# Performance work log

Hardware: AMD Instinct MI355X
Metric: run time of the kernel (lower is better)

## Reference

```python
import jax, jax.numpy as jnp
import numpy as np

# SigNet forward: time-augment -> depth-3 path signature (basepoint=True, via
# Chen's identity over per-segment tensor exponentials) -> Linear. dropout p=0.

B, L, CIN, OUT = 256, 256, 8, 128
C = CIN + 1                      # +1 time channel from signatory.Augment
SIG_CH = C + C**2 + C**3         # signatory.signature_channels(C, depth=3) = 819


def setup_inputs() -> dict:
    key = jax.random.key(0)
    k1, k2, k3 = jax.random.split(key, 3)
    inp = jax.random.normal(k1, (B, L, CIN), dtype=jnp.float32)
    W = jax.random.normal(k2, (SIG_CH, OUT), dtype=jnp.float32) / np.sqrt(SIG_CH).astype(np.float32)
    b = jax.random.normal(k3, (OUT,), dtype=jnp.float32) * 0.01
    return {"inp": inp, "W": W, "b": b}


def _chen(a, bb):
    # Chen's identity for truncated tensor algebra (depth 3):
    # (a*b)_k = sum_{i+j=k} a_i (x) b_j  (with a_0 = b_0 = 1)
    a1, a2, a3 = a
    b1, b2, b3 = bb
    c1 = a1 + b1
    c2 = a2 + b2 + jnp.einsum('...i,...j->...ij', a1, b1)
    c3 = (a3 + b3
          + jnp.einsum('...ij,...k->...ijk', a2, b1)
          + jnp.einsum('...i,...jk->...ijk', a1, b2))
    return (c1, c2, c3)


def _signature_depth3(path):
    # path: [B, L, C]; basepoint=True -> prepend the zero point before diffing
    Bn, Ln, Cn = path.shape
    path = jnp.concatenate([jnp.zeros((Bn, 1, Cn), path.dtype), path], axis=1)
    dx = jnp.moveaxis(jnp.diff(path, axis=1), 1, 0)  # [L, B, C] increments
    # Tensor exponential of each linear segment: exp(dx)_k = dx^{(x)k} / k!
    e1 = dx
    e2 = 0.5 * jnp.einsum('lbi,lbj->lbij', dx, dx)
    e3 = jnp.einsum('lbij,lbk->lbijk', e2, dx) / 3.0  # = dx^(x)3 / 6
    s1, s2, s3 = jax.lax.associative_scan(_chen, (e1, e2, e3), axis=0)
    return jnp.concatenate([s1[-1].reshape(Bn, -1),
                            s2[-1].reshape(Bn, -1),
                            s3[-1].reshape(Bn, -1)], axis=-1)  # [B, SIG_CH]


def reference(inp, W, b):
    Bn, Ln, _ = inp.shape
    # signatory.Augment include_time: linspace(0,1,L) channel, placed first
    t = jnp.broadcast_to(jnp.linspace(0.0, 1.0, Ln, dtype=inp.dtype)[None, :, None], (Bn, Ln, 1))
    x = jnp.concatenate([t, inp], axis=-1)  # [B, L, C]
    y = _signature_depth3(x)
    return y @ W + b  # dropout p=0 is identity
```

## Files before the change

kernel.cpp:

```cpp
#include <hip/hip_runtime.h>


#define PAD 260

__global__ __launch_bounds__(512) void signet_fwd(
    const float* __restrict__ inp,
    const float* __restrict__ W,
    const float* __restrict__ bias,
    float* __restrict__ out)
{
    __shared__ __align__(16) float Wt[9][PAD];
    __shared__ __align__(16) float Zt[9][PAD];
    __shared__ __align__(16) float Dt[9][PAD];
    __shared__ __align__(16) float Xt[9][PAD];
    __shared__ float sig[820];
    __shared__ __align__(16) float4 pbuf[16][32];
    __shared__ __align__(16) float4 part3[244];

    const int tid = threadIdx.x;
    const int b   = blockIdx.x;

    {
        const int t = tid & 255;
        const float* rc = inp + (size_t)b * 2048 + (size_t)t * 8;
        if (tid < 256) {
            float4 c0 = *(const float4*)rc;
            float4 p0 = make_float4(0.f, 0.f, 0.f, 0.f);
            float  tp = 0.f;
            if (t > 0) { p0 = *(const float4*)(rc - 8); tp = (float)(t - 1) * (1.0f / 255.0f); }
            float cur[5] = { (float)t * (1.0f / 255.0f), c0.x, c0.y, c0.z, c0.w };
            float prv[5] = { tp, p0.x, p0.y, p0.z, p0.w };
            if (t == 0) cur[0] = 0.0f;
            #pragma unroll
            for (int c = 0; c < 5; ++c) {
                const float d = cur[c] - prv[c];
                Dt[c][t] = d;
                Xt[c][t] = cur[c];
                Wt[c][t] = prv[c] + 0.5f * d;
                Zt[c][t] = 0.5f * prv[c] + d * (1.0f / 6.0f);
            }
        } else {
            float4 c1 = *(const float4*)(rc + 4);
            float4 p1 = make_float4(0.f, 0.f, 0.f, 0.f);
            if (t > 0) p1 = *(const float4*)(rc - 4);
            float cur[4] = { c1.x, c1.y, c1.z, c1.w };
            float prv[4] = { p1.x, p1.y, p1.z, p1.w };
            #pragma unroll
            for (int c = 0; c < 4; ++c) {
                const float d = cur[c] - prv[c];
                Dt[5 + c][t] = d;
                Xt[5 + c][t] = cur[c];
                Wt[5 + c][t] = prv[c] + 0.5f * d;
                Zt[5 + c][t] = 0.5f * prv[c] + d * (1.0f / 6.0f);
            }
        }
    }
    __syncthreads();

    const int  half = tid >> 8;
    const int  lt   = tid & 255;
    const bool own3 = (lt < 243);
    const int  pp = lt / 3;
    const int  mm = lt - pp * 3;
    const int  si = pp / 9;
    const int  sj = pp - si * 9;
    const int  sk = mm * 3;

    float a0 = 0.f, a1 = 0.f, a2 = 0.f, s2a = 0.f;

    if (own3) {
        const int qb = half * 32;
        const float4* w4 = (const float4*)Wt[si] + qb;
        const float4* z4 = (const float4*)Zt[si] + qb;
        const float4* dj = (const float4*)Dt[sj] + qb;
        const float4* x0 = (const float4*)Xt[sk] + qb;
        const float4* x1 = (const float4*)Xt[sk + 1] + qb;
        const float4* x2 = (const float4*)Xt[sk + 2] + qb;
        const float4* d0 = (const float4*)Dt[sk] + qb;
        const float4* d1 = (const float4*)Dt[sk + 1] + qb;
        const float4* d2 = (const float4*)Dt[sk + 2] + qb;

        #pragma unroll 2
        for (int q = 0; q < 32; ++q) {
            const float4 w = w4[q], z = z4[q], dd = dj[q];
            const float4 X0 = x0[q], X1 = x1[q], X2 = x2[q];
            const float4 D0 = d0[q], D1 = d1[q], D2 = d2[q];
            {   const float u = w.x * dd.x, v = z.x * dd.x;  s2a += u;
                a0 = fmaf(v, D0.x, fmaf(-u, X0.x, a0));
                a1 = fmaf(v, D1.x, fmaf(-u, X1.x, a1));
                a2 = fmaf(v, D2.x, fmaf(-u, X2.x, a2)); }
            {   const float u = w.y * dd.y, v = z.y * dd.y;  s2a += u;
                a0 = fmaf(v, D0.y, fmaf(-u, X0.y, a0));
                a1 = fmaf(v, D1.y, fmaf(-u, X1.y, a1));
                a2 = fmaf(v, D2.y, fmaf(-u, X2.y, a2)); }
            {   const float u = w.z * dd.z, v = z.z * dd.z;  s2a += u;
                a0 = fmaf(v, D0.z, fmaf(-u, X0.z, a0));
                a1 = fmaf(v, D1.z, fmaf(-u, X1.z, a1));
                a2 = fmaf(v, D2.z, fmaf(-u, X2.z, a2)); }
            {   const float u = w.w * dd.w, v = z.w * dd.w;  s2a += u;
                a0 = fmaf(v, D0.w, fmaf(-u, X0.w, a0));
                a1 = fmaf(v, D1.w, fmaf(-u, X1.w, a1));
                a2 = fmaf(v, D2.w, fmaf(-u, X2.w, a2)); }
        }
    }

    if (own3 && half) part3[lt] = make_float4(a0, a1, a2, s2a);
    __syncthreads();

    if (own3 && !half) {
        const float4 p = part3[lt];
        a0 += p.x;  a1 += p.y;  a2 += p.z;  s2a += p.w;
        const float xl0 = Xt[sk][255], xl1 = Xt[sk + 1][255], xl2 = Xt[sk + 2][255];
        a0 = fmaf(s2a, xl0, a0);
        a1 = fmaf(s2a, xl1, a1);
        a2 = fmaf(s2a, xl2, a2);
        const int base = 90 + pp * 9 + sk;
        sig[base]     = a0;
        sig[base + 1] = a1;
        sig[base + 2] = a2;
        if (mm == 0) sig[9 + pp] = s2a;
    }
    if (tid < 9) sig[tid] = Xt[tid][255];
    __syncthreads();

    {
        const int oq = tid & 31;
        const int sl = tid >> 5;
        float4 acc = make_float4(0.f, 0.f, 0.f, 0.f);
        const float4* W4 = (const float4*)W;
        for (int ch = sl; ch < 819; ch += 16) {
            const float s = sig[ch];
            const float4 wv = W4[(size_t)ch * 32 + oq];
            acc.x = fmaf(s, wv.x, acc.x);
            acc.y = fmaf(s, wv.y, acc.y);
            acc.z = fmaf(s, wv.z, acc.z);
            acc.w = fmaf(s, wv.w, acc.w);
        }
        pbuf[sl][oq] = acc;
    }
    __syncthreads();
    if (tid < 32) {
        float4 r = pbuf[0][tid];
        #pragma unroll
        for (int s = 1; s < 16; ++s) {
            const float4 p = pbuf[s][tid];
            r.x += p.x; r.y += p.y; r.z += p.z; r.w += p.w;
        }
        const float4 bv = ((const float4*)bias)[tid];
        r.x += bv.x; r.y += bv.y; r.z += bv.z; r.w += bv.w;
        ((float4*)(out + (size_t)b * 128))[tid] = r;
    }
}

extern "C" void kernel_launch(void* const* d_in, const int* in_sizes, int n_in,
                              void* d_out, int out_size, void* d_ws, size_t ws_size,
                              hipStream_t stream) {
    const float* inp  = (const float*)d_in[0];
    const float* Wp   = (const float*)d_in[1];
    const float* bias = (const float*)d_in[2];
    float* outp = (float*)d_out;
    (void)in_sizes; (void)n_in; (void)out_size; (void)d_ws; (void)ws_size;

    hipLaunchKernelGGL(signet_fwd, dim3(256), dim3(512), 0, stream,
                       inp, Wp, bias, outp);
}
```

Baseline: 19.50 us.

## Repartition depth-3 signature work into time chunks with register-blocked j accumulators

Replaces the per-(i,j,k-triple) thread mapping, where each of 243 thread pairs streamed all 256 timesteps, with 16 time chunks of 16 steps. Each of 27 threads per chunk handles one (i, k-triple) and keeps 27+9 register accumulators over all j. The Z and X arrays are no longer stored in shared memory; they are recomputed from W and D, and shared memory is unioned for the partial sums and the linear-layer reduction. The goal is to reuse shared-memory loads across j and cut LDS traffic, at the cost of higher register pressure and an extra cross-chunk reduction pass over 729+81 outputs.

```diff
diff --git a/kernel.cpp b/kernel.cpp
--- a/kernel.cpp
+++ b/kernel.cpp
@@ -1,21 +1,24 @@
 #include <hip/hip_runtime.h>
 
 
-#define PAD 260
+#define ROWF   260
+#define NCHUNK 16
+#define TPC    27
+#define ASTRIDE 29
+#define PART_S2_OFF (NCHUNK * TPC * ASTRIDE)
+#define UNION_FLOATS (PART_S2_OFF + NCHUNK * 81)
 
 __global__ __launch_bounds__(512) void signet_fwd(
     const float* __restrict__ inp,
-    const float* __restrict__ W,
+    const float* __restrict__ Wg,
     const float* __restrict__ bias,
     float* __restrict__ out)
 {
-    __shared__ __align__(16) float Wt[9][PAD];
-    __shared__ __align__(16) float Zt[9][PAD];
-    __shared__ __align__(16) float Dt[9][PAD];
-    __shared__ __align__(16) float Xt[9][PAD];
     __shared__ float sig[820];
-    __shared__ __align__(16) float4 pbuf[16][32];
-    __shared__ __align__(16) float4 part3[244];
+    __shared__ __align__(16) float u[UNION_FLOATS];
+
+    float* Wt = u;
+    float* Dt = u + 9 * ROWF;
 
     const int tid = threadIdx.x;
     const int b   = blockIdx.x;
@@ -30,14 +33,11 @@
             if (t > 0) { p0 = *(const float4*)(rc - 8); tp = (float)(t - 1) * (1.0f / 255.0f); }
             float cur[5] = { (float)t * (1.0f / 255.0f), c0.x, c0.y, c0.z, c0.w };
             float prv[5] = { tp, p0.x, p0.y, p0.z, p0.w };
-            if (t == 0) cur[0] = 0.0f;
             #pragma unroll
             for (int c = 0; c < 5; ++c) {
                 const float d = cur[c] - prv[c];
-                Dt[c][t] = d;
-                Xt[c][t] = cur[c];
-                Wt[c][t] = prv[c] + 0.5f * d;
-                Zt[c][t] = 0.5f * prv[c] + d * (1.0f / 6.0f);
+                Dt[c * ROWF + t] = d;
+                Wt[c * ROWF + t] = prv[c] + 0.5f * d;
             }
         } else {
             float4 c1 = *(const float4*)(rc + 4);
@@ -48,102 +48,147 @@
             #pragma unroll
             for (int c = 0; c < 4; ++c) {
                 const float d = cur[c] - prv[c];
-                Dt[5 + c][t] = d;
-                Xt[5 + c][t] = cur[c];
-                Wt[5 + c][t] = prv[c] + 0.5f * d;
-                Zt[5 + c][t] = 0.5f * prv[c] + d * (1.0f / 6.0f);
+                Dt[(5 + c) * ROWF + t] = d;
+                Wt[(5 + c) * ROWF + t] = prv[c] + 0.5f * d;
             }
         }
     }
     __syncthreads();
 
-    const int  half = tid >> 8;
-    const int  lt   = tid & 255;
-    const bool own3 = (lt < 243);
-    const int  pp = lt / 3;
-    const int  mm = lt - pp * 3;
-    const int  si = pp / 9;
-    const int  sj = pp - si * 9;
-    const int  sk = mm * 3;
-
-    float a0 = 0.f, a1 = 0.f, a2 = 0.f, s2a = 0.f;
-
-    if (own3) {
-        const int qb = half * 32;
-        const float4* w4 = (const float4*)Wt[si] + qb;
-        const float4* z4 = (const float4*)Zt[si] + qb;
-        const float4* dj = (const float4*)Dt[sj] + qb;
-        const float4* x0 = (const float4*)Xt[sk] + qb;
-        const float4* x1 = (const float4*)Xt[sk + 1] + qb;
-        const float4* x2 = (const float4*)Xt[sk + 2] + qb;
-        const float4* d0 = (const float4*)Dt[sk] + qb;
-        const float4* d1 = (const float4*)Dt[sk + 1] + qb;
-        const float4* d2 = (const float4*)Dt[sk + 2] + qb;
-
-        #pragma unroll 2
-        for (int q = 0; q < 32; ++q) {
-            const float4 w = w4[q], z = z4[q], dd = dj[q];
-            const float4 X0 = x0[q], X1 = x1[q], X2 = x2[q];
-            const float4 D0 = d0[q], D1 = d1[q], D2 = d2[q];
-            {   const float u = w.x * dd.x, v = z.x * dd.x;  s2a += u;
-                a0 = fmaf(v, D0.x, fmaf(-u, X0.x, a0));
-                a1 = fmaf(v, D1.x, fmaf(-u, X1.x, a1));
-                a2 = fmaf(v, D2.x, fmaf(-u, X2.x, a2)); }
-            {   const float u = w.y * dd.y, v = z.y * dd.y;  s2a += u;
-                a0 = fmaf(v, D0.y, fmaf(-u, X0.y, a0));
-                a1 = fmaf(v, D1.y, fmaf(-u, X1.y, a1));
-                a2 = fmaf(v, D2.y, fmaf(-u, X2.y, a2)); }
-            {   const float u = w.z * dd.z, v = z.z * dd.z;  s2a += u;
-                a0 = fmaf(v, D0.z, fmaf(-u, X0.z, a0));
-                a1 = fmaf(v, D1.z, fmaf(-u, X1.z, a1));
-                a2 = fmaf(v, D2.z, fmaf(-u, X2.z, a2)); }
-            {   const float u = w.w * dd.w, v = z.w * dd.w;  s2a += u;
-                a0 = fmaf(v, D0.w, fmaf(-u, X0.w, a0));
-                a1 = fmaf(v, D1.w, fmaf(-u, X1.w, a1));
-                a2 = fmaf(v, D2.w, fmaf(-u, X2.w, a2)); }
-        }
-    }
-
-    if (own3 && half) part3[lt] = make_float4(a0, a1, a2, s2a);
-    __syncthreads();
-
-    if (own3 && !half) {
-        const float4 p = part3[lt];
-        a0 += p.x;  a1 += p.y;  a2 += p.z;  s2a += p.w;
-        const float xl0 = Xt[sk][255], xl1 = Xt[sk + 1][255], xl2 = Xt[sk + 2][255];
-        a0 = fmaf(s2a, xl0, a0);
-        a1 = fmaf(s2a, xl1, a1);
-        a2 = fmaf(s2a, xl2, a2);
-        const int base = 90 + pp * 9 + sk;
-        sig[base]     = a0;
-        sig[base + 1] = a1;
-        sig[base + 2] = a2;
-        if (mm == 0) sig[9 + pp] = s2a;
-    }
-    if (tid < 9) sig[tid] = Xt[tid][255];
+    const int  chunk = tid / TPC;
+    const int  tloc  = tid - chunk * TPC;
+    const int  ci    = tloc / 3;
+    const int  kt    = tloc - ci * 3;
+    const bool act   = (chunk < NCHUNK);
+
+    float a[9][3];
+    float s2a[9];
+    #pragma unroll
+    for (int j = 0; j < 9; ++j) { s2a[j] = 0.f; a[j][0] = 0.f; a[j][1] = 0.f; a[j][2] = 0.f; }
+
+    if (act) {
+        const int fb = chunk * 4;
+        const float4* W4 = (const float4*)u;
+        const float4* D4 = (const float4*)u + 9 * 65;
+        const int k0 = 3 * kt;
+
+        #pragma unroll
+        for (int q = 0; q < 4; ++q) {
+            const float4 w  = W4[ci * 65 + fb + q];
+            const float4 di = D4[ci * 65 + fb + q];
+            const float4 Wk0 = W4[(k0 + 0) * 65 + fb + q];
+            const float4 Wk1 = W4[(k0 + 1) * 65 + fb + q];
+            const float4 Wk2 = W4[(k0 + 2) * 65 + fb + q];
+            const float4 Dk0 = D4[(k0 + 0) * 65 + fb + q];
+            const float4 Dk1 = D4[(k0 + 1) * 65 + fb + q];
+            const float4 Dk2 = D4[(k0 + 2) * 65 + fb + q];
+
+            float4 z, X0, X1, X2;
+            z.x = fmaf(-(1.0f / 12.0f), di.x, 0.5f * w.x);
+            z.y = fmaf(-(1.0f / 12.0f), di.y, 0.5f * w.y);
+            z.z = fmaf(-(1.0f / 12.0f), di.z, 0.5f * w.z);
+            z.w = fmaf(-(1.0f / 12.0f), di.w, 0.5f * w.w);
+            X0.x = fmaf(0.5f, Dk0.x, Wk0.x); X0.y = fmaf(0.5f, Dk0.y, Wk0.y);
+            X0.z = fmaf(0.5f, Dk0.z, Wk0.z); X0.w = fmaf(0.5f, Dk0.w, Wk0.w);
+            X1.x = fmaf(0.5f, Dk1.x, Wk1.x); X1.y = fmaf(0.5f, Dk1.y, Wk1.y);
+            X1.z = fmaf(0.5f, Dk1.z, Wk1.z); X1.w = fmaf(0.5f, Dk1.w, Wk1.w);
+            X2.x = fmaf(0.5f, Dk2.x, Wk2.x); X2.y = fmaf(0.5f, Dk2.y, Wk2.y);
+            X2.z = fmaf(0.5f, Dk2.z, Wk2.z); X2.w = fmaf(0.5f, Dk2.w, Wk2.w);
+
+            #pragma unroll
+            for (int j = 0; j < 9; ++j) {
+                const float4 dj = D4[j * 65 + fb + q];
+                { const float uu = w.x * dj.x, vv = z.x * dj.x; s2a[j] += uu;
+                  a[j][0] = fmaf(vv, Dk0.x, fmaf(-uu, X0.x, a[j][0]));
+                  a[j][1] = fmaf(vv, Dk1.x, fmaf(-uu, X1.x, a[j][1]));
+                  a[j][2] = fmaf(vv, Dk2.x, fmaf(-uu, X2.x, a[j][2])); }
+                { const float uu = w.y * dj.y, vv = z.y * dj.y; s2a[j] += uu;
+                  a[j][0] = fmaf(vv, Dk0.y, fmaf(-uu, X0.y, a[j][0]));
+                  a[j][1] = fmaf(vv, Dk1.y, fmaf(-uu, X1.y, a[j][1]));
+                  a[j][2] = fmaf(vv, Dk2.y, fmaf(-uu, X2.y, a[j][2])); }
+                { const float uu = w.z * dj.z, vv = z.z * dj.z; s2a[j] += uu;
+                  a[j][0] = fmaf(vv, Dk0.z, fmaf(-uu, X0.z, a[j][0]));
+                  a[j][1] = fmaf(vv, Dk1.z, fmaf(-uu, X1.z, a[j][1]));
+                  a[j][2] = fmaf(vv, Dk2.z, fmaf(-uu, X2.z, a[j][2])); }
+                { const float uu = w.w * dj.w, vv = z.w * dj.w; s2a[j] += uu;
+                  a[j][0] = fmaf(vv, Dk0.w, fmaf(-uu, X0.w, a[j][0]));
+                  a[j][1] = fmaf(vv, Dk1.w, fmaf(-uu, X1.w, a[j][1]));
+                  a[j][2] = fmaf(vv, Dk2.w, fmaf(-uu, X2.w, a[j][2])); }
+            }
+        }
+    }
+    __syncthreads();
+
+    if (tid < 9) {
+        const float wl = Wt[tid * ROWF + 255];
+        const float dl = Dt[tid * ROWF + 255];
+        sig[tid] = fmaf(0.5f, dl, wl);
+    }
+    __syncthreads();
+
+    if (act) {
+        float* pa = u + (chunk * TPC + tloc) * ASTRIDE;
+        #pragma unroll
+        for (int j = 0; j < 9; ++j) {
+            pa[j * 3 + 0] = a[j][0];
+            pa[j * 3 + 1] = a[j][1];
+            pa[j * 3 + 2] = a[j][2];
+        }
+        if (kt == 0) {
+            float* ps = u + PART_S2_OFF + chunk * 81 + ci * 9;
+            #pragma unroll
+            for (int j = 0; j < 9; ++j) ps[j] = s2a[j];
+        }
+    }
+    __syncthreads();
+
+    if (tid < 81) {
+        float s = 0.f;
+        #pragma unroll
+        for (int c = 0; c < NCHUNK; ++c) s += u[PART_S2_OFF + c * 81 + tid];
+        sig[9 + tid] = s;
+    }
+    __syncthreads();
+
+    for (int e = tid; e < 729; e += 512) {
+        const int i  = e / 81;
+        const int r  = e - i * 81;
+        const int j  = r / 9;
+        const int k  = r - j * 9;
+        const int ktv = k / 3;
+        const int km  = k - ktv * 3;
+        const int toff = (i * 3 + ktv) * ASTRIDE + j * 3 + km;
+        float s = 0.f;
+        #pragma unroll
+        for (int c = 0; c < NCHUNK; ++c) s += u[c * (TPC * ASTRIDE) + toff];
+        s = fmaf(sig[9 + i * 9 + j], sig[k], s);
+        sig[90 + e] = s;
+    }
     __syncthreads();
 
     {
         const int oq = tid & 31;
         const int sl = tid >> 5;
         float4 acc = make_float4(0.f, 0.f, 0.f, 0.f);
-        const float4* W4 = (const float4*)W;
+        const float4* Wq = (const float4*)Wg;
         for (int ch = sl; ch < 819; ch += 16) {
             const float s = sig[ch];
-            const float4 wv = W4[(size_t)ch * 32 + oq];
+            const float4 wv = Wq[(size_t)ch * 32 + oq];
             acc.x = fmaf(s, wv.x, acc.x);
             acc.y = fmaf(s, wv.y, acc.y);
             acc.z = fmaf(s, wv.z, acc.z);
             acc.w = fmaf(s, wv.w, acc.w);
         }
-        pbuf[sl][oq] = acc;
+        float4* pbuf = (float4*)u;
+        pbuf[sl * 32 + oq] = acc;
     }
     __syncthreads();
     if (tid < 32) {
-        float4 r = pbuf[0][tid];
+        const float4* pbuf = (const float4*)u;
+        float4 r = pbuf[tid];
         #pragma unroll
         for (int s = 1; s < 16; ++s) {
-            const float4 p = pbuf[s][tid];
+            const float4 p = pbuf[s * 32 + tid];
             r.x += p.x; r.y += p.y; r.z += p.z; r.w += p.w;
         }
         const float4 bv = ((const float4*)bias)[tid];
```

New measurement: 18.25 us. -6.4%, faster.
